# Performance work log

Hardware: AMD Instinct MI355X
Metric: run time of the kernel (lower is better)

Reference implementation:

```python
import jax, jax.numpy as jnp
import numpy as np

EPS = 1e-6

def _rms(x, scale):
    # flax nn.RMSNorm: x / sqrt(mean(x^2)+eps) * scale, no mean subtraction
    return x * scale * jax.lax.rsqrt(jnp.mean(x * x, axis=-1, keepdims=True) + EPS)


def _forward(x, mem_k, mem_v, norm1_scale, norm2_scale,
             Wq, bq, Wk, bk, Wv, bv, Wz, bz,
             Wgz, bgz, Wgh, bgh,
             Wg1, bg1, Wg2, bg2, Wgc1, bgc1, Wgc2, bgc2,
             Awq, abq, Awk, abk, Awv, abv, Awo, abo,
             Wf1, bf1, Wf2, bf2):
    B, S, D = x.shape
    M = mem_k.shape[1]
    H = 8
    hd = D // H

    x_norm = _rms(x, norm1_scale)
    q = x_norm @ Wq + bq
    k = x_norm @ Wk + bk
    v = x_norm @ Wv + bv
    z = x_norm @ Wz + bz

    # input-dependent decay gamma in (1e-6, 1-1e-6)
    gamma_base = jax.nn.sigmoid(jax.nn.gelu(z @ Wg1 + bg1) @ Wg2 + bg2)
    gamma_mod = jax.nn.sigmoid(jax.nn.gelu(k @ Wgc1 + bgc1) @ Wgc2 + bgc2)
    gamma = jnp.clip(gamma_base * gamma_mod, 1e-6, 1.0 - 1e-6)

    # gated leaky recurrence over sequence: h depends on W_g_h(h_prev) -> strict scan
    def step(h_prev, zt_gt):
        z_t, g_t = zt_gt  # [B, D] each
        gate = jax.nn.sigmoid(z_t @ Wgz + bgz + h_prev @ Wgh + bgh)
        h_tilde = (1.0 - gate) * h_prev + gate * z_t
        h_t = h_tilde + g_t * h_prev
        return h_t, h_t

    h0 = jnp.zeros((B, D), dtype=x.dtype)
    z_T = jnp.swapaxes(z, 0, 1)          # [S, B, D]
    gamma_T = jnp.swapaxes(gamma, 0, 1)  # [S, B, D]
    _, h_seq_T = jax.lax.scan(step, h0, (z_T, gamma_T))
    h_seq = jnp.swapaxes(h_seq_T, 0, 1)  # [B, S, D]

    # MultiMemoryAttention: q from q_input, K/V from memory state banks [B, M, D]
    qh = (q @ Awq + abq).reshape(B, S, H, hd)
    kh = (mem_k @ Awk + abk).reshape(B, M, H, hd)
    vh = (mem_v @ Awv + abv).reshape(B, M, H, hd)
    scores = jnp.einsum('bshd,bmhd->bhsm', qh, kh) / jnp.sqrt(jnp.asarray(hd, x.dtype))
    probs = jax.nn.softmax(scores, axis=-1)
    mem_out = jnp.einsum('bhsm,bmhd->bshd', probs, vh).reshape(B, S, D) @ Awo + abo

    combined = h_seq + mem_out + v * 0.1
    x_res = x + combined  # dropout deterministic (training=False)

    x_norm2 = _rms(x_res, norm2_scale)
    ffn = jax.nn.gelu(x_norm2 @ Wf1 + bf1) @ Wf2 + bf2
    return x_res + ffn


def setup_inputs() -> dict:
    key = jax.random.key(0)
    B, S, D, H, F, M = 4, 4096, 1024, 8, 4096, 512
    Dq = D // 4
    ks = jax.random.split(key, 24)
    def w(i, shape):
        return jax.random.normal(ks[i], shape, dtype=jnp.float32) * 0.02
    d = {
        'x': jax.random.normal(ks[0], (B, S, D), dtype=jnp.float32),
        'mem_k': jax.random.normal(ks[1], (B, M, D), dtype=jnp.float32),
        'mem_v': jax.random.normal(ks[2], (B, M, D), dtype=jnp.float32),
        'norm1_scale': jnp.ones((D,), jnp.float32),
        'norm2_scale': jnp.ones((D,), jnp.float32),
        'Wq': w(3, (D, D)), 'bq': jnp.zeros((D,), jnp.float32),
        'Wk': w(4, (D, D)), 'bk': jnp.zeros((D,), jnp.float32),
        'Wv': w(5, (D, D)), 'bv': jnp.zeros((D,), jnp.float32),
        'Wz': w(6, (D, D)), 'bz': jnp.zeros((D,), jnp.float32),
        'Wgz': w(7, (D, D)), 'bgz': jnp.zeros((D,), jnp.float32),
        'Wgh': w(8, (D, D)), 'bgh': jnp.zeros((D,), jnp.float32),
        'Wg1': w(9, (D, Dq)), 'bg1': jnp.zeros((Dq,), jnp.float32),
        'Wg2': w(10, (Dq, D)), 'bg2': jnp.zeros((D,), jnp.float32),
        'Wgc1': w(11, (D, Dq)), 'bgc1': jnp.zeros((Dq,), jnp.float32),
        'Wgc2': w(12, (Dq, D)), 'bgc2': jnp.zeros((D,), jnp.float32),
        'Awq': w(13, (D, D)), 'abq': jnp.zeros((D,), jnp.float32),
        'Awk': w(14, (D, D)), 'abk': jnp.zeros((D,), jnp.float32),
        'Awv': w(15, (D, D)), 'abv': jnp.zeros((D,), jnp.float32),
        'Awo': w(16, (D, D)), 'abo': jnp.zeros((D,), jnp.float32),
        'Wf1': w(17, (D, F)), 'bf1': jnp.zeros((F,), jnp.float32),
        'Wf2': w(18, (F, D)), 'bf2': jnp.zeros((D,), jnp.float32),
    }
    return d


def reference(x, mem_k, mem_v, norm1_scale, norm2_scale,
              Wq, bq, Wk, bk, Wv, bv, Wz, bz,
              Wgz, bgz, Wgh, bgh,
              Wg1, bg1, Wg2, bg2, Wgc1, bgc1, Wgc2, bgc2,
              Awq, abq, Awk, abk, Awv, abv, Awo, abo,
              Wf1, bf1, Wf2, bf2):
    return _forward(x, mem_k, mem_v, norm1_scale, norm2_scale,
                    Wq, bq, Wk, bk, Wv, bv, Wz, bz,
                    Wgz, bgz, Wgh, bgh,
                    Wg1, bg1, Wg2, bg2, Wgc1, bgc1, Wgc2, bgc2,
                    Awq, abq, Awk, abk, Awv, abv, Awo, abo,
                    Wf1, bf1, Wf2, bf2)
```

## Files before the change

### kernel.cpp

```cpp
#include <hip/hip_runtime.h>
#include <stdint.h>

typedef short s16x8 __attribute__((ext_vector_type(8)));
typedef float f32x4 __attribute__((ext_vector_type(4)));
typedef uint  u32x4 __attribute__((ext_vector_type(4)));

#define DEV static __device__ __forceinline__

DEV float bf2f(ushort u){ union{uint i;float f;}v; v.i=((uint)u)<<16; return v.f; }
DEV ushort f2bf(float f){ union{float f;uint i;}v; v.f=f; return (ushort)((v.i + 0x7FFFu + ((v.i>>16)&1u))>>16); }
DEV float fsigmoid(float x){ return 1.f/(1.f+__expf(-x)); }
DEV float fgelu(float x){
  float u = 0.7978845608028654f*(x + 0.044715f*x*x*x);
  float e = __expf(2.f*u);
  float th = 1.f - 2.f/(e+1.f);
  return 0.5f*x*(1.f+th);
}
DEV f32x4 mfma16(s16x8 a, s16x8 b, f32x4 c){
  return __builtin_amdgcn_mfma_f32_16x16x32_bf16(a,b,c,0,0,0);
}

DEV void store_u64_coherent(unsigned long long* p, unsigned long long v){
  asm volatile("global_store_dwordx2 %0, %1, off sc0 sc1" :: "v"(p), "v"(v) : "memory");
}
DEV void load8_u64_coherent(const unsigned long long* p, u32x4& r0, u32x4& r1,
                            u32x4& r2, u32x4& r3){
  asm volatile("global_load_dwordx4 %0, %4, off sc0 sc1\n\t"
               "global_load_dwordx4 %1, %4, off offset:16 sc0 sc1\n\t"
               "global_load_dwordx4 %2, %4, off offset:32 sc0 sc1\n\t"
               "global_load_dwordx4 %3, %4, off offset:48 sc0 sc1\n\t"
               "s_waitcnt vmcnt(0)"
               : "=&v"(r0), "=&v"(r1), "=&v"(r2), "=&v"(r3)
               : "v"(p) : "memory");
}

__global__ __launch_bounds__(256) void transpose_cvt(const float* __restrict__ src,
                                                     ushort* __restrict__ dst, int K, int N){
  __shared__ float tile[64][65];
  int tk = blockIdx.y*64, tn = blockIdx.x*64;
  int t = threadIdx.x;
  int c4 = (t & 15)*4, r0 = t >> 4;
  #pragma unroll
  for (int p=0;p<4;++p){
    int r = r0 + p*16;
    float4 v = *(const float4*)(src + (size_t)(tk+r)*N + tn + c4);
    tile[r][c4+0]=v.x; tile[r][c4+1]=v.y; tile[r][c4+2]=v.z; tile[r][c4+3]=v.w;
  }
  __syncthreads();
  #pragma unroll
  for (int p=0;p<4;++p){
    int n = r0 + p*16;
    ushort4 o = make_ushort4(f2bf(tile[c4+0][n]), f2bf(tile[c4+1][n]),
                             f2bf(tile[c4+2][n]), f2bf(tile[c4+3][n]));
    *(ushort4*)(dst + (size_t)(tn+n)*K + tk + c4) = o;
  }
}

__global__ __launch_bounds__(256) void cvt_bf16(const float* __restrict__ s,
                                                ushort* __restrict__ d, int n){
  int i = (blockIdx.x*256 + threadIdx.x)*4;
  if (i < n){
    float4 v = *(const float4*)(s + i);
    ushort4 o = make_ushort4(f2bf(v.x), f2bf(v.y), f2bf(v.z), f2bf(v.w));
    *(ushort4*)(d + i) = o;
  }
}

__global__ __launch_bounds__(256) void bias_sum_k(const float* __restrict__ a,
                                                  const float* __restrict__ b,
                                                  float* __restrict__ o){
  int i = blockIdx.x*256 + threadIdx.x;
  if (i < 1024) o[i] = a[i] + b[i];
}

__global__ __launch_bounds__(256) void fuse_bias(const float* __restrict__ b_in,
                                                 const float* __restrict__ W,
                                                 const float* __restrict__ b_out,
                                                 float* __restrict__ o, int K, int N){
  int n = blockIdx.x*256 + threadIdx.x;
  if (n < N){
    float s = b_out[n];
    for (int k=0;k<K;++k) s += b_in[k]*W[(size_t)k*N + n];
    o[n] = s;
  }
}

__global__ __launch_bounds__(256) void rms_kernel(const float* __restrict__ x,
                                                  const float* __restrict__ scale,
                                                  ushort* __restrict__ out){
  int row = blockIdx.x, t = threadIdx.x;
  const float* xr = x + (size_t)row*1024;
  float4 v = *(const float4*)(xr + t*4);
  float ss = v.x*v.x + v.y*v.y + v.z*v.z + v.w*v.w;
  #pragma unroll
  for (int o=1;o<64;o<<=1) ss += __shfl_xor(ss, o);
  __shared__ float wsum[4];
  if ((t & 63)==0) wsum[t>>6] = ss;
  __syncthreads();
  float tot = wsum[0]+wsum[1]+wsum[2]+wsum[3];
  float rstd = rsqrtf(tot*(1.f/1024.f) + 1e-6f);
  float4 sc = *(const float4*)(scale + t*4);
  ushort4 o4 = make_ushort4(f2bf(v.x*sc.x*rstd), f2bf(v.y*sc.y*rstd),
                            f2bf(v.z*sc.z*rstd), f2bf(v.w*sc.w*rstd));
  *(ushort4*)(out + (size_t)row*1024 + t*4) = o4;
}

template<int EPI>
__global__ __launch_bounds__(256,2) void gemm_bf16(
    const ushort* __restrict__ A, const ushort* __restrict__ Bt,
    const float* __restrict__ bias, void* __restrict__ Cout,
    const void* __restrict__ aux0, const void* __restrict__ aux1,
    int M, int N, int K)
{
  __shared__ ushort Al[128*32];
  __shared__ ushort Bl[128*32];
  const int t = threadIdx.x, ln = t & 63;
  const int m0 = blockIdx.y*128, n0 = blockIdx.x*128;
  const int wv = t >> 6, wr = wv >> 1, wc = wv & 1;
  const int lr = ln & 15, lk = ln >> 4;
  f32x4 acc[4][4] = {};
  for (int kk = 0; kk < K; kk += 32) {
    #pragma unroll
    for (int cc = 0; cc < 2; ++cc) {
      int e = cc*256 + t;
      int r = e >> 2, sg = e & 3;
      __builtin_amdgcn_global_load_lds((const uint*)(A  + (size_t)(m0+r)*K + kk + sg*8),
                                       (uint*)&Al[e*8], 16, 0, 0);
      __builtin_amdgcn_global_load_lds((const uint*)(Bt + (size_t)(n0+r)*K + kk + sg*8),
                                       (uint*)&Bl[e*8], 16, 0, 0);
    }
    __syncthreads();
    s16x8 af[4], bfr[4];
    #pragma unroll
    for (int m=0;m<4;++m) af[m]  = *(const s16x8*)&Al[(wr*64 + m*16 + lr)*32 + lk*8];
    #pragma unroll
    for (int n=0;n<4;++n) bfr[n] = *(const s16x8*)&Bl[(wc*64 + n*16 + lr)*32 + lk*8];
    #pragma unroll
    for (int m=0;m<4;++m)
      #pragma unroll
      for (int n=0;n<4;++n)
        acc[m][n] = mfma16(af[m], bfr[n], acc[m][n]);
    __syncthreads();
  }
  #pragma unroll
  for (int m=0;m<4;++m){
    #pragma unroll
    for (int n=0;n<4;++n){
      #pragma unroll
      for (int j=0;j<4;++j){
        int row = m0 + wr*64 + m*16 + lk*4 + j;
        int col = n0 + wc*64 + n*16 + lr;
        float v = acc[m][n][j] + (bias ? bias[col] : 0.f);
        size_t idx = (size_t)row*N + col;
        if constexpr (EPI==0){ ((ushort*)Cout)[idx] = f2bf(v); }
        else if constexpr (EPI==1){ ((ushort*)Cout)[idx] = f2bf(fgelu(v)); }
        else if constexpr (EPI==2){ ((ushort*)Cout)[idx] = f2bf(fsigmoid(v)); }
        else if constexpr (EPI==3){
          float g = fsigmoid(v) * bf2f(((const ushort*)aux0)[idx]);
          g = fminf(fmaxf(g, 1e-6f), 1.f-1e-6f);
          ((ushort*)Cout)[idx] = f2bf(g);
        }
        else if constexpr (EPI==4){
          float o = v + ((const float*)aux0)[idx] + 0.1f*bf2f(((const ushort*)aux1)[idx]);
          ((float*)Cout)[idx] = o;
        }
        else if constexpr (EPI==5){ ((float*)Cout)[idx] += v; }
        else if constexpr (EPI==6){
          int bb = row >> 9, mm = row & 511, hh = col >> 7, dd = col & 127;
          ((ushort*)Cout)[ (((size_t)(bb*8 + hh)*128 + dd) << 9) + mm ] = f2bf(v);
        }
        else if constexpr (EPI==7){
          ((ushort*)Cout)[(size_t)col*M + row] = f2bf(v);
        }
      }
    }
  }
}

__global__ __launch_bounds__(256,1) void attn_kernel(
  const ushort* __restrict__ qh, const ushort* __restrict__ kh,
  const ushort* __restrict__ vhT, ushort* __restrict__ att)
{
  __shared__ ushort P[4*16*512];
  const int t = threadIdx.x, ln = t & 63, wv = t >> 6;
  const int lr = ln & 15, lk = ln >> 4;
  const int b = blockIdx.z, h = blockIdx.y, s0 = blockIdx.x*64;

  const ushort* qrow = qh + (size_t)(b*4096 + s0 + wv*16 + lr)*1024 + h*128 + lk*8;
  s16x8 qf[4];
  #pragma unroll
  for (int kt=0;kt<4;++kt) qf[kt] = *(const s16x8*)(qrow + kt*32);
  __syncthreads();

  f32x4 zero4 = {0.f,0.f,0.f,0.f};
  f32x4 sacc[32];
  #pragma unroll
  for (int i=0;i<32;++i) sacc[i] = zero4;

  const ushort* kbase = kh + (size_t)(b*512)*1024 + h*128 + lk*8;
  #pragma unroll
  for (int mt=0;mt<32;++mt){
    const ushort* krow = kbase + (size_t)(mt*16 + lr)*1024;
    #pragma unroll
    for (int kt=0;kt<4;++kt){
      s16x8 kf = *(const s16x8*)(krow + kt*32);
      sacc[mt] = mfma16(qf[kt], kf, sacc[mt]);
    }
  }
  const float scale = 0.08838834764831845f;
  float inv[4];
  #pragma unroll
  for (int j=0;j<4;++j){
    float m = -3.4e38f;
    #pragma unroll
    for (int mt=0;mt<32;++mt) m = fmaxf(m, sacc[mt][j]);
    m = fmaxf(m, __shfl_xor(m,1)); m = fmaxf(m, __shfl_xor(m,2));
    m = fmaxf(m, __shfl_xor(m,4)); m = fmaxf(m, __shfl_xor(m,8));
    float s = 0.f;
    #pragma unroll
    for (int mt=0;mt<32;++mt){
      float p = __expf((sacc[mt][j]-m)*scale);
      sacc[mt][j] = p; s += p;
    }
    s += __shfl_xor(s,1); s += __shfl_xor(s,2);
    s += __shfl_xor(s,4); s += __shfl_xor(s,8);
    inv[j] = 1.f/s;
  }
  char* pb = (char*)P + wv*16384;
  #pragma unroll
  for (int j=0;j<4;++j){
    int row = lk*4 + j;
    uint xr = (uint)((row & 7) << 4);
    #pragma unroll
    for (int mt=0;mt<32;++mt){
      int col = mt*16 + lr;
      *(ushort*)(pb + row*1024 + (((uint)(col*2)) ^ xr)) = f2bf(sacc[mt][j]);
    }
  }
  f32x4 oacc[8];
  #pragma unroll
  for (int i=0;i<8;++i) oacc[i] = zero4;
  const ushort* vb = vhT + (size_t)(b*8 + h)*128*512;
  const char* prow = (char*)P + wv*16384 + lr*1024;
  uint xrr = (uint)((lr & 7) << 4);
  #pragma unroll
  for (int km=0;km<16;++km){
    s16x8 pf = *(const s16x8*)(prow + (((uint)((km*32 + lk*8)*2)) ^ xrr));
    #pragma unroll
    for (int dt=0;dt<8;++dt){
      s16x8 vf = *(const s16x8*)(vb + (size_t)(dt*16 + lr)*512 + km*32 + lk*8);
      oacc[dt] = mfma16(pf, vf, oacc[dt]);
    }
  }
  ushort* ob = att + (size_t)(b*4096 + s0 + wv*16)*1024 + h*128;
  #pragma unroll
  for (int dt=0;dt<8;++dt){
    #pragma unroll
    for (int j=0;j<4;++j){
      int row = lk*4 + j, col = dt*16 + lr;
      ob[(size_t)row*1024 + col] = f2bf(oacc[dt][j]*inv[j]);
    }
  }
}

#define SCAN_NB 64
__global__ __launch_bounds__(256,1) void scan_kernel(
  const float* __restrict__ Wgh,
  const ushort* __restrict__ u_bf, const ushort* __restrict__ z_bf,
  const ushort* __restrict__ g_bf, float* __restrict__ xres,
  unsigned long long* __restrict__ h_buf)
{
  __shared__ ushort WL[16*1032];
  __shared__ ushort HL[5*1032];
  __shared__ float  red[4][16][4];
  const int t = threadIdx.x, blk = blockIdx.x;
  const int ln = t & 63, wv = t >> 6;

  {
    const int c = t & 15, i0q = (t >> 4) * 64;
    for (int j = 0; j < 64; ++j) {
      int i = i0q + j;
      WL[c*1032 + i] = f2bf(Wgh[(size_t)i*1024 + blk*16 + c]);
    }
  }
  for (int e = t; e < 1032; e += 256) HL[4*1032 + e] = 0;

  float hmine = 0.f;
  const int c_ep = t & 15, b_ep = t >> 4;
  float uu=0.f, zz=0.f, gg=0.f, xv=0.f;
  if (t < 64) {
    size_t i0 = ((size_t)(b_ep*4096))*1024 + blk*16 + c_ep;
    uu = bf2f(u_bf[i0]); zz = bf2f(z_bf[i0]); gg = bf2f(g_bf[i0]); xv = xres[i0];
  }
  __syncthreads();

  const int arow = ln & 15, akc = ln >> 4;
  const ushort* Abase = &HL[(arow < 4 ? arow : 4)*1032 + akc*8];
  const ushort* Bbase = &WL[(ln & 15)*1032 + akc*8];
  const int hb_t = t >> 6, hk0 = (t & 63)*16;

  for (int step = 0; step < 4096; ++step) {
    {
      const unsigned long long* hs = h_buf + (size_t)(step & 1)*2048 + t*8;
      u32x4 r0, r1, r2, r3;
      while (true) {
        load8_u64_coherent(hs, r0, r1, r2, r3);
        uint st = (uint)step;
        if (r0.y==st && r0.w==st && r1.y==st && r1.w==st &&
            r2.y==st && r2.w==st && r3.y==st && r3.w==st) break;
      }
      uint* dst = (uint*)&HL[hb_t*1032 + hk0];
      *(uint4*)(dst + 0) = make_uint4(r0.x, r0.z, r1.x, r1.z);
      *(uint4*)(dst + 4) = make_uint4(r2.x, r2.z, r3.x, r3.z);
    }
    __syncthreads();
    f32x4 acc = {0.f,0.f,0.f,0.f};
    #pragma unroll
    for (int m = 0; m < 8; ++m) {
      int koff = wv*256 + m*32;
      s16x8 a = *(const s16x8*)(Abase + koff);
      s16x8 b = *(const s16x8*)(Bbase + koff);
      acc = mfma16(a, b, acc);
    }
    if (ln < 16) *(f32x4*)&red[wv][ln][0] = acc;
    __syncthreads();
    if (t < 64) {
      float y = red[0][c_ep][b_ep] + red[1][c_ep][b_ep]
              + red[2][c_ep][b_ep] + red[3][c_ep][b_ep];
      float gate = fsigmoid(y + uu);
      float hn = hmine + gate*(zz - hmine) + gg*hmine;
      hmine = hn;
      int colg = blk*16 + c_ep;
      float hup = __shfl_down(hn, 1);
      if ((t & 1) == 0) {
        unsigned long long pk = ((unsigned long long)(uint)(step+1) << 32)
                              | ((uint)f2bf(hup) << 16) | (uint)f2bf(hn);
        store_u64_coherent(h_buf + (size_t)((step+1)&1)*2048 + b_ep*512 + (colg>>1), pk);
      }
      size_t idx = ((size_t)(b_ep*4096 + step))*1024 + colg;
      xres[idx] = xv + hn;
      int sn = (step+1 < 4096) ? step+1 : 4095;
      size_t idxn = ((size_t)(b_ep*4096 + sn))*1024 + colg;
      uu = bf2f(u_bf[idxn]); zz = bf2f(z_bf[idxn]); gg = bf2f(g_bf[idxn]);
      xv = xres[idxn];
    }
  }
}

extern "C" void kernel_launch(void* const* d_in, const int* in_sizes, int n_in,
                              void* d_out, int out_size, void* d_ws, size_t ws_size,
                              hipStream_t stream)
{
  const float* x    = (const float*)d_in[0];
  const float* memk = (const float*)d_in[1];
  const float* memv = (const float*)d_in[2];
  const float* n1s  = (const float*)d_in[3];
  const float* n2s  = (const float*)d_in[4];
  const float* Wq = (const float*)d_in[5];   const float* bq = (const float*)d_in[6];
  const float* Wk = (const float*)d_in[7];   const float* bk = (const float*)d_in[8];
  const float* Wv = (const float*)d_in[9];   const float* bv = (const float*)d_in[10];
  const float* Wz = (const float*)d_in[11];  const float* bz = (const float*)d_in[12];
  const float* Wgz = (const float*)d_in[13]; const float* bgz = (const float*)d_in[14];
  const float* Wgh = (const float*)d_in[15]; const float* bgh = (const float*)d_in[16];
  const float* Wg1 = (const float*)d_in[17]; const float* bg1 = (const float*)d_in[18];
  const float* Wg2 = (const float*)d_in[19]; const float* bg2 = (const float*)d_in[20];
  const float* Wgc1 = (const float*)d_in[21]; const float* bgc1 = (const float*)d_in[22];
  const float* Wgc2 = (const float*)d_in[23]; const float* bgc2 = (const float*)d_in[24];
  const float* Awq = (const float*)d_in[25]; const float* abq = (const float*)d_in[26];
  const float* Awk = (const float*)d_in[27]; const float* abk = (const float*)d_in[28];
  const float* Awv = (const float*)d_in[29]; const float* abv = (const float*)d_in[30];
  const float* Awo = (const float*)d_in[31]; const float* abo = (const float*)d_in[32];
  const float* Wf1 = (const float*)d_in[33]; const float* bf1 = (const float*)d_in[34];
  const float* Wf2 = (const float*)d_in[35]; const float* bf2 = (const float*)d_in[36];
  (void)in_sizes; (void)n_in; (void)out_size; (void)ws_size;

  char* ws = (char*)d_ws;
  constexpr size_t MB = 1ull<<20;
  ushort* WvT     = (ushort*)(ws + 0*MB);
  ushort* WzT     = (ushort*)(ws + 2*MB);
  ushort* WgzT    = (ushort*)(ws + 4*MB);
  ushort* WqAwqT  = (ushort*)(ws + 6*MB);
  ushort* AwkT    = (ushort*)(ws + 8*MB);
  ushort* AwvT    = (ushort*)(ws + 10*MB);
  ushort* AwoT    = (ushort*)(ws + 12*MB);
  ushort* Wf1T    = (ushort*)(ws + 14*MB);
  ushort* Wf2Tc   = (ushort*)(ws + 22*MB);
  ushort* Wg1T    = (ushort*)(ws + 30*MB);
  ushort* Wg2T    = (ushort*)(ws + 30*MB + 512*1024);
  ushort* Wgc2T   = (ushort*)(ws + 31*MB);
  ushort* WkWgc1T = (ushort*)(ws + 31*MB + 512*1024);
  float* bsum = (float*)(ws + 32*MB);
  float* bqh  = (float*)(ws + 32*MB + 4096);
  float* bkg  = (float*)(ws + 32*MB + 8192);
  char*  scanB = ws + 32*MB + 65536;
  ushort* Abuf = (ushort*)(ws + 33*MB);
  ushort* Bbuf = (ushort*)(ws + 65*MB);
  ushort* Cbuf = (ushort*)(ws + 97*MB);
  ushort* Dbuf = (ushort*)(ws + 129*MB);
  ushort* Ebuf = (ushort*)(ws + 161*MB);
  char* db = (char*)d_out;
  ushort* t1B   = (ushort*)(db + 0);
  ushort* memkB = (ushort*)(db + 8*MB);
  ushort* memvB = (ushort*)(db + 12*MB);
  ushort* khB   = (ushort*)(db + 16*MB);
  ushort* vhTB  = (ushort*)(db + 20*MB);
  ushort* gbB   = (ushort*)(db + 24*MB);
  ushort* WtmpB = (ushort*)(db + 56*MB);
  ushort* BtTB  = (ushort*)(db + 58*MB);

  const int M1 = 16384;
  dim3 b256(256);
  auto T = [&](const float* s, ushort* d, int K, int N){
    transpose_cvt<<<dim3(N/64, K/64), b256, 0, stream>>>(s, d, K, N);
  };
  #define G(EPI, Ap, Bp, bi, Cp, a0, a1, Mv, Nv, Kv) \
    gemm_bf16<EPI><<<dim3((Nv)/128,(Mv)/128), b256, 0, stream>>>( \
      (const ushort*)(Ap), (const ushort*)(Bp), bi, (void*)(Cp), a0, a1, Mv, Nv, Kv)

  cvt_bf16<<<1024, b256, 0, stream>>>(Wq, WtmpB, 1048576);
  T(Awq, BtTB, 1024, 1024);
  G(7, WtmpB, BtTB, nullptr, WqAwqT, nullptr, nullptr, 1024, 1024, 1024);
  fuse_bias<<<4, b256, 0, stream>>>(bq, Awq, abq, bqh, 1024, 1024);
  cvt_bf16<<<1024, b256, 0, stream>>>(Wk, WtmpB, 1048576);
  T(Wgc1, BtTB, 1024, 256);
  G(7, WtmpB, BtTB, nullptr, WkWgc1T, nullptr, nullptr, 1024, 256, 1024);
  fuse_bias<<<1, b256, 0, stream>>>(bk, Wgc1, bgc1, bkg, 1024, 256);
  T(Wv,WvT,1024,1024); T(Wz,WzT,1024,1024); T(Wgz,WgzT,1024,1024);
  T(Wg1,Wg1T,1024,256); T(Wg2,Wg2T,256,1024); T(Wgc2,Wgc2T,256,1024);
  T(Awk,AwkT,1024,1024); T(Awv,AwvT,1024,1024); T(Awo,AwoT,1024,1024);
  T(Wf1,Wf1T,1024,4096);
  for (int cch = 0; cch < 4; ++cch)
    T(Wf2 + (size_t)cch*1048576, Wf2Tc + (size_t)cch*1048576, 1024, 1024);
  bias_sum_k<<<4, b256, 0, stream>>>(bgz, bgh, bsum);
  cvt_bf16<<<2048, b256, 0, stream>>>(memk, memkB, 2097152);
  cvt_bf16<<<2048, b256, 0, stream>>>(memv, memvB, 2097152);

  rms_kernel<<<M1, b256, 0, stream>>>(x, n1s, Abuf);
  G(0, Abuf, WzT, bz, Bbuf, nullptr, nullptr, M1, 1024, 1024);
  G(0, Abuf, WvT, bv, Cbuf, nullptr, nullptr, M1, 1024, 1024);
  G(0, Abuf, WqAwqT, bqh, Dbuf, nullptr, nullptr, M1, 1024, 1024);
  G(0, Bbuf, WgzT, bsum, Ebuf, nullptr, nullptr, M1, 1024, 1024);
  G(1, Bbuf, Wg1T, bg1, t1B, nullptr, nullptr, M1, 256, 1024);
  G(2, t1B, Wg2T, bg2, gbB, nullptr, nullptr, M1, 1024, 256);
  G(1, Abuf, WkWgc1T, bkg, t1B, nullptr, nullptr, M1, 256, 1024);
  G(3, t1B, Wgc2T, bgc2, Abuf, gbB, nullptr, M1, 1024, 256);
  G(0, memkB, AwkT, abk, khB, nullptr, nullptr, 2048, 1024, 1024);
  G(6, memvB, AwvT, abv, vhTB, nullptr, nullptr, 2048, 1024, 1024);
  attn_kernel<<<dim3(64,8,4), b256, 0, stream>>>(Dbuf, khB, vhTB, Dbuf);
  G(4, Dbuf, AwoT, abo, d_out, (const void*)x, (const void*)Cbuf, M1, 1024, 1024);
  hipMemsetAsync(scanB, 0, 32768, stream);
  scan_kernel<<<SCAN_NB, b256, 0, stream>>>(Wgh, Ebuf, Bbuf, Abuf, (float*)d_out,
                                            (unsigned long long*)scanB);
  rms_kernel<<<M1, b256, 0, stream>>>((const float*)d_out, n2s, Cbuf);
  for (int cch = 0; cch < 4; ++cch) {
    G(1, Cbuf, Wf1T + (size_t)cch*1048576, bf1 + cch*1024, Dbuf, nullptr, nullptr, M1, 1024, 1024);
    G(5, Dbuf, Wf2Tc + (size_t)cch*1048576, (cch==0 ? bf2 : nullptr), d_out, nullptr, nullptr, M1, 1024, 1024);
  }
  #undef G
}
```

Baseline: 12.04 ms.

## Fuse FFN into scan kernel with worker blocks consuming finished rows

Merges the sequential recurrence scan, the second RMSNorm and the two FFN GEMMs into one persistent launch. The first 64 blocks run the scan as before. The extra blocks take 32-row tiles from an atomic work queue, poll the scan's step counters until those rows are done, then compute norm, FFN and residual in place. This is meant to hide the FFN and norm time behind the latency-bound scan. In exchange, the scan now uses coherent stores, the FFN tiles read weights straight from global memory rather than through a tuned GEMM, and the spin-waiting blocks may compete with the scan for memory bandwidth.

Measured after the change: 12.93 ms. 1.07x slower.

```diff
diff --git a/kernel.cpp b/kernel.cpp
--- a/kernel.cpp
+++ b/kernel.cpp
@@ -22,6 +22,9 @@
 
 DEV void store_u64_coherent(unsigned long long* p, unsigned long long v){
   asm volatile("global_store_dwordx2 %0, %1, off sc0 sc1" :: "v"(p), "v"(v) : "memory");
+}
+DEV void store_f32_coherent(float* p, float v){
+  asm volatile("global_store_dword %0, %1, off sc0 sc1" :: "v"(p), "v"(v) : "memory");
 }
 DEV void load8_u64_coherent(const unsigned long long* p, u32x4& r0, u32x4& r1,
                             u32x4& r2, u32x4& r3){
@@ -32,6 +35,27 @@
                "s_waitcnt vmcnt(0)"
                : "=&v"(r0), "=&v"(r1), "=&v"(r2), "=&v"(r3)
                : "v"(p) : "memory");
+}
+DEV unsigned long long load_u64_coherent(const unsigned long long* p){
+  unsigned long long v;
+  asm volatile("global_load_dwordx2 %0, %1, off sc0 sc1\n\ts_waitcnt vmcnt(0)"
+               : "=v"(v) : "v"(p) : "memory");
+  return v;
+}
+DEV void load8x16_coh(const float* p, f32x4 r[8]){
+  asm volatile(
+    "global_load_dwordx4 %0, %8, off sc0 sc1\n\t"
+    "global_load_dwordx4 %1, %8, off offset:16 sc0 sc1\n\t"
+    "global_load_dwordx4 %2, %8, off offset:32 sc0 sc1\n\t"
+    "global_load_dwordx4 %3, %8, off offset:48 sc0 sc1\n\t"
+    "global_load_dwordx4 %4, %8, off offset:64 sc0 sc1\n\t"
+    "global_load_dwordx4 %5, %8, off offset:80 sc0 sc1\n\t"
+    "global_load_dwordx4 %6, %8, off offset:96 sc0 sc1\n\t"
+    "global_load_dwordx4 %7, %8, off offset:112 sc0 sc1\n\t"
+    "s_waitcnt vmcnt(0)"
+    : "=&v"(r[0]), "=&v"(r[1]), "=&v"(r[2]), "=&v"(r[3]),
+      "=&v"(r[4]), "=&v"(r[5]), "=&v"(r[6]), "=&v"(r[7])
+    : "v"(p) : "memory");
 }
 
 __global__ __launch_bounds__(256) void transpose_cvt(const float* __restrict__ src,
@@ -264,86 +288,225 @@
 }
 
 #define SCAN_NB 64
-__global__ __launch_bounds__(256,1) void scan_kernel(
+__global__ __launch_bounds__(256,1) void scan_ffn_kernel(
   const float* __restrict__ Wgh,
   const ushort* __restrict__ u_bf, const ushort* __restrict__ z_bf,
   const ushort* __restrict__ g_bf, float* __restrict__ xres,
-  unsigned long long* __restrict__ h_buf)
+  unsigned long long* __restrict__ h_buf, uint* __restrict__ queue,
+  const ushort* __restrict__ Wf1T, const ushort* __restrict__ Wf2Tc,
+  const float* __restrict__ bf1, const float* __restrict__ bf2,
+  const float* __restrict__ n2s)
 {
-  __shared__ ushort WL[16*1032];
-  __shared__ ushort HL[5*1032];
-  __shared__ float  red[4][16][4];
-  const int t = threadIdx.x, blk = blockIdx.x;
-  const int ln = t & 63, wv = t >> 6;
-
-  {
-    const int c = t & 15, i0q = (t >> 4) * 64;
-    for (int j = 0; j < 64; ++j) {
-      int i = i0q + j;
-      WL[c*1032 + i] = f2bf(Wgh[(size_t)i*1024 + blk*16 + c]);
-    }
-  }
-  for (int e = t; e < 1032; e += 256) HL[4*1032 + e] = 0;
-
-  float hmine = 0.f;
-  const int c_ep = t & 15, b_ep = t >> 4;
-  float uu=0.f, zz=0.f, gg=0.f, xv=0.f;
-  if (t < 64) {
-    size_t i0 = ((size_t)(b_ep*4096))*1024 + blk*16 + c_ep;
-    uu = bf2f(u_bf[i0]); zz = bf2f(z_bf[i0]); gg = bf2f(g_bf[i0]); xv = xres[i0];
-  }
-  __syncthreads();
-
-  const int arow = ln & 15, akc = ln >> 4;
-  const ushort* Abase = &HL[(arow < 4 ? arow : 4)*1032 + akc*8];
-  const ushort* Bbase = &WL[(ln & 15)*1032 + akc*8];
-  const int hb_t = t >> 6, hk0 = (t & 63)*16;
-
-  for (int step = 0; step < 4096; ++step) {
+  __shared__ __align__(16) char SM[132352];
+  const int t = threadIdx.x;
+
+  if (blockIdx.x < SCAN_NB) {
+    ushort* WL = (ushort*)SM;
+    ushort* HL = (ushort*)(SM + 33024);
+    float (*red)[16][4] = (float(*)[16][4])(SM + 43344);
+    const int blk = blockIdx.x, ln = t & 63, wv = t >> 6;
     {
-      const unsigned long long* hs = h_buf + (size_t)(step & 1)*2048 + t*8;
-      u32x4 r0, r1, r2, r3;
+      const int c = t & 15, i0q = (t >> 4) * 64;
+      for (int j = 0; j < 64; ++j) {
+        int i = i0q + j;
+        WL[c*1032 + i] = f2bf(Wgh[(size_t)i*1024 + blk*16 + c]);
+      }
+    }
+    for (int e = t; e < 1032; e += 256) HL[4*1032 + e] = 0;
+
+    float hmine = 0.f;
+    const int c_ep = t & 15, b_ep = t >> 4;
+    float uu=0.f, zz=0.f, gg=0.f, xv=0.f;
+    if (t < 64) {
+      size_t i0 = ((size_t)(b_ep*4096))*1024 + blk*16 + c_ep;
+      uu = bf2f(u_bf[i0]); zz = bf2f(z_bf[i0]); gg = bf2f(g_bf[i0]); xv = xres[i0];
+    }
+    __syncthreads();
+
+    const int arow = ln & 15, akc = ln >> 4;
+    const ushort* Abase = &HL[(arow < 4 ? arow : 4)*1032 + akc*8];
+    const ushort* Bbase = &WL[(ln & 15)*1032 + akc*8];
+    const int hb_t = t >> 6, hk0 = (t & 63)*16;
+
+    for (int step = 0; step < 4096; ++step) {
+      {
+        const unsigned long long* hs = h_buf + (size_t)(step & 1)*2048 + t*8;
+        u32x4 r0, r1, r2, r3;
+        while (true) {
+          load8_u64_coherent(hs, r0, r1, r2, r3);
+          uint st = (uint)step;
+          if (r0.y==st && r0.w==st && r1.y==st && r1.w==st &&
+              r2.y==st && r2.w==st && r3.y==st && r3.w==st) break;
+        }
+        uint* dst = (uint*)&HL[hb_t*1032 + hk0];
+        *(uint4*)(dst + 0) = make_uint4(r0.x, r0.z, r1.x, r1.z);
+        *(uint4*)(dst + 4) = make_uint4(r2.x, r2.z, r3.x, r3.z);
+      }
+      __syncthreads();
+      f32x4 acc = {0.f,0.f,0.f,0.f};
+      #pragma unroll
+      for (int m = 0; m < 8; ++m) {
+        int koff = wv*256 + m*32;
+        s16x8 a = *(const s16x8*)(Abase + koff);
+        s16x8 b = *(const s16x8*)(Bbase + koff);
+        acc = mfma16(a, b, acc);
+      }
+      if (ln < 16) *(f32x4*)&red[wv][ln][0] = acc;
+      __syncthreads();
+      if (t < 64) {
+        float y = red[0][c_ep][b_ep] + red[1][c_ep][b_ep]
+                + red[2][c_ep][b_ep] + red[3][c_ep][b_ep];
+        float gate = fsigmoid(y + uu);
+        float hn = hmine + gate*(zz - hmine) + gg*hmine;
+        hmine = hn;
+        int colg = blk*16 + c_ep;
+        float hup = __shfl_down(hn, 1);
+        if ((t & 1) == 0) {
+          unsigned long long pk = ((unsigned long long)(uint)(step+1) << 32)
+                                | ((uint)f2bf(hup) << 16) | (uint)f2bf(hn);
+          store_u64_coherent(h_buf + (size_t)((step+1)&1)*2048 + b_ep*512 + (colg>>1), pk);
+        }
+        size_t idx = ((size_t)(b_ep*4096 + step))*1024 + colg;
+        store_f32_coherent(&xres[idx], xv + hn);
+        int sn = (step+1 < 4096) ? step+1 : 4095;
+        size_t idxn = ((size_t)(b_ep*4096 + sn))*1024 + colg;
+        uu = bf2f(u_bf[idxn]); zz = bf2f(z_bf[idxn]); gg = bf2f(g_bf[idxn]);
+        xv = xres[idxn];
+      }
+    }
+    asm volatile("s_waitcnt vmcnt(0)" ::: "memory");
+    if (t < 64 && (t & 1) == 0) {
+      store_u64_coherent(h_buf + (size_t)b_ep*512 + blk*8 + (c_ep>>1), 4098ULL << 32);
+    }
+    return;
+  }
+
+  ushort* Aq = (ushort*)SM;
+  ushort* Fq = (ushort*)(SM + 66048);
+  float*  XT = (float*)SM;
+  int* tileslot = (int*)(SM + 132096);
+  const int ln = t & 63, w = t >> 6;
+  const int lr = ln & 15, lk = ln >> 4;
+
+  for (;;) {
+    if (t == 0) *tileslot = (int)atomicAdd(queue, 1u);
+    __syncthreads();
+    const int tk = *tileslot;
+    __syncthreads();
+    if (tk >= 512) break;
+    const int s0 = (tk >> 2)*32, b = tk & 3;
+    const size_t rowbase = (size_t)b*4096 + s0;
+
+    if (w == 0) {
+      const int vt = s0 + 34;
+      const unsigned long long* pw = h_buf + (size_t)b*512 + ln*8;
       while (true) {
-        load8_u64_coherent(hs, r0, r1, r2, r3);
-        uint st = (uint)step;
-        if (r0.y==st && r0.w==st && r1.y==st && r1.w==st &&
-            r2.y==st && r2.w==st && r3.y==st && r3.w==st) break;
-      }
-      uint* dst = (uint*)&HL[hb_t*1032 + hk0];
-      *(uint4*)(dst + 0) = make_uint4(r0.x, r0.z, r1.x, r1.z);
-      *(uint4*)(dst + 4) = make_uint4(r2.x, r2.z, r3.x, r3.z);
-    }
-    __syncthreads();
-    f32x4 acc = {0.f,0.f,0.f,0.f};
-    #pragma unroll
-    for (int m = 0; m < 8; ++m) {
-      int koff = wv*256 + m*32;
-      s16x8 a = *(const s16x8*)(Abase + koff);
-      s16x8 b = *(const s16x8*)(Bbase + koff);
-      acc = mfma16(a, b, acc);
-    }
-    if (ln < 16) *(f32x4*)&red[wv][ln][0] = acc;
-    __syncthreads();
-    if (t < 64) {
-      float y = red[0][c_ep][b_ep] + red[1][c_ep][b_ep]
-              + red[2][c_ep][b_ep] + red[3][c_ep][b_ep];
-      float gate = fsigmoid(y + uu);
-      float hn = hmine + gate*(zz - hmine) + gg*hmine;
-      hmine = hn;
-      int colg = blk*16 + c_ep;
-      float hup = __shfl_down(hn, 1);
-      if ((t & 1) == 0) {
-        unsigned long long pk = ((unsigned long long)(uint)(step+1) << 32)
-                              | ((uint)f2bf(hup) << 16) | (uint)f2bf(hn);
-        store_u64_coherent(h_buf + (size_t)((step+1)&1)*2048 + b_ep*512 + (colg>>1), pk);
-      }
-      size_t idx = ((size_t)(b_ep*4096 + step))*1024 + colg;
-      xres[idx] = xv + hn;
-      int sn = (step+1 < 4096) ? step+1 : 4095;
-      size_t idxn = ((size_t)(b_ep*4096 + sn))*1024 + colg;
-      uu = bf2f(u_bf[idxn]); zz = bf2f(z_bf[idxn]); gg = bf2f(g_bf[idxn]);
-      xv = xres[idxn];
-    }
+        unsigned long long v = load_u64_coherent(pw);
+        if (__all((int)((uint)(v >> 32) >= (uint)vt))) break;
+        __builtin_amdgcn_s_sleep(8);
+      }
+    }
+    __syncthreads();
+
+    {
+      const int r8 = t >> 3, p8 = t & 7;
+      const float* xrow = xres + (rowbase + r8)*1024 + p8*128;
+      f32x4 va[4][8];
+      load8x16_coh(xrow +  0, va[0]);
+      load8x16_coh(xrow + 32, va[1]);
+      load8x16_coh(xrow + 64, va[2]);
+      load8x16_coh(xrow + 96, va[3]);
+      float ss = 0.f;
+      #pragma unroll
+      for (int g=0; g<4; ++g)
+        #pragma unroll
+        for (int i=0; i<8; ++i)
+          ss += va[g][i][0]*va[g][i][0] + va[g][i][1]*va[g][i][1]
+              + va[g][i][2]*va[g][i][2] + va[g][i][3]*va[g][i][3];
+      ss += __shfl_xor(ss,1); ss += __shfl_xor(ss,2); ss += __shfl_xor(ss,4);
+      float rstd = rsqrtf(ss*(1.f/1024.f) + 1e-6f);
+      #pragma unroll
+      for (int g=0; g<4; ++g)
+        #pragma unroll
+        for (int i=0; i<8; ++i) {
+          int c = p8*128 + g*32 + i*4;
+          float4 sc4 = *(const float4*)(n2s + c);
+          ushort4 o4 = make_ushort4(f2bf(va[g][i][0]*sc4.x*rstd),
+                                    f2bf(va[g][i][1]*sc4.y*rstd),
+                                    f2bf(va[g][i][2]*sc4.z*rstd),
+                                    f2bf(va[g][i][3]*sc4.w*rstd));
+          *(ushort4*)&Aq[r8*1032 + c] = o4;
+        }
+    }
+    __syncthreads();
+
+    f32x4 acc2[2][16] = {};
+    for (int nc = 0; nc < 4; ++nc) {
+      f32x4 acc1[2][16] = {};
+      const ushort* Bp1 = Wf1T + ((size_t)(nc*1024 + w*256 + lr))*1024 + lk*8;
+      for (int kk = 0; kk < 32; ++kk) {
+        s16x8 a0 = *(const s16x8*)&Aq[lr*1032 + kk*32 + lk*8];
+        s16x8 a1 = *(const s16x8*)&Aq[(16+lr)*1032 + kk*32 + lk*8];
+        #pragma unroll
+        for (int ct = 0; ct < 16; ++ct) {
+          s16x8 bf = *(const s16x8*)(Bp1 + (size_t)ct*16*1024 + kk*32);
+          acc1[0][ct] = mfma16(a0, bf, acc1[0][ct]);
+          acc1[1][ct] = mfma16(a1, bf, acc1[1][ct]);
+        }
+      }
+      #pragma unroll
+      for (int ct = 0; ct < 16; ++ct) {
+        int colc = w*256 + ct*16 + lr;
+        float bb = bf1[nc*1024 + colc];
+        #pragma unroll
+        for (int rg = 0; rg < 2; ++rg)
+          #pragma unroll
+          for (int j = 0; j < 4; ++j) {
+            int rowl = rg*16 + lk*4 + j;
+            Fq[rowl*1032 + colc] = f2bf(fgelu(acc1[rg][ct][j] + bb));
+          }
+      }
+      __syncthreads();
+      const ushort* Bp2 = Wf2Tc + (size_t)nc*1048576 + ((size_t)(w*256 + lr))*1024 + lk*8;
+      for (int kk = 0; kk < 32; ++kk) {
+        s16x8 a0 = *(const s16x8*)&Fq[lr*1032 + kk*32 + lk*8];
+        s16x8 a1 = *(const s16x8*)&Fq[(16+lr)*1032 + kk*32 + lk*8];
+        #pragma unroll
+        for (int ot = 0; ot < 16; ++ot) {
+          s16x8 bf = *(const s16x8*)(Bp2 + (size_t)ot*16*1024 + kk*32);
+          acc2[0][ot] = mfma16(a0, bf, acc2[0][ot]);
+          acc2[1][ot] = mfma16(a1, bf, acc2[1][ot]);
+        }
+      }
+      __syncthreads();
+    }
+
+    {
+      const int r8 = t >> 3, p8 = t & 7;
+      const float* xrow = xres + (rowbase + r8)*1024 + p8*128;
+      #pragma unroll
+      for (int g=0; g<4; ++g) {
+        f32x4 vb[8];
+        load8x16_coh(xrow + g*32, vb);
+        #pragma unroll
+        for (int i=0; i<8; ++i)
+          *(f32x4*)&XT[r8*1024 + p8*128 + g*32 + i*4] = vb[i];
+      }
+    }
+    __syncthreads();
+    #pragma unroll
+    for (int ot = 0; ot < 16; ++ot) {
+      int col = w*256 + ot*16 + lr;
+      float bb = bf2[col];
+      #pragma unroll
+      for (int rg = 0; rg < 2; ++rg)
+        #pragma unroll
+        for (int j = 0; j < 4; ++j) {
+          int rowl = rg*16 + lk*4 + j;
+          xres[(rowbase + rowl)*1024 + col] = XT[rowl*1024 + col] + bb + acc2[rg][ot][j];
+        }
+    }
+    __syncthreads();
   }
 }
 
@@ -448,13 +611,10 @@
   G(6, memvB, AwvT, abv, vhTB, nullptr, nullptr, 2048, 1024, 1024);
   attn_kernel<<<dim3(64,8,4), b256, 0, stream>>>(Dbuf, khB, vhTB, Dbuf);
   G(4, Dbuf, AwoT, abo, d_out, (const void*)x, (const void*)Cbuf, M1, 1024, 1024);
-  hipMemsetAsync(scanB, 0, 32768, stream);
-  scan_kernel<<<SCAN_NB, b256, 0, stream>>>(Wgh, Ebuf, Bbuf, Abuf, (float*)d_out,
-                                            (unsigned long long*)scanB);
-  rms_kernel<<<M1, b256, 0, stream>>>((const float*)d_out, n2s, Cbuf);
-  for (int cch = 0; cch < 4; ++cch) {
-    G(1, Cbuf, Wf1T + (size_t)cch*1048576, bf1 + cch*1024, Dbuf, nullptr, nullptr, M1, 1024, 1024);
-    G(5, Dbuf, Wf2Tc + (size_t)cch*1048576, (cch==0 ? bf2 : nullptr), d_out, nullptr, nullptr, M1, 1024, 1024);
-  }
+  hipMemsetAsync(scanB, 0, 36864, stream);
+  scan_ffn_kernel<<<256, b256, 0, stream>>>(Wgh, Ebuf, Bbuf, Abuf, (float*)d_out,
+                                            (unsigned long long*)scanB,
+                                            (uint*)(scanB + 32768),
+                                            Wf1T, Wf2Tc, bf1, bf2, n2s);
   #undef G
 }
```
